# Optimization experiments

Hardware: AMD Instinct MI355X
Metric: run time of the kernel (lower is better)

Reference implementation:

```python
import jax, jax.numpy as jnp
import numpy as np

B, N, D = 8, 1024, 768
R, SH = 10, 2
H = R + SH            # 12 total heads
DH = D // H           # 64
DF = 2 * D            # FFN hidden


def _layernorm(x, g, b, eps=1e-5):
    mu = jnp.mean(x, axis=-1, keepdims=True)
    var = jnp.var(x, axis=-1, keepdims=True)
    return (x - mu) * jax.lax.rsqrt(var + eps) * g + b


def setup_inputs() -> dict:
    key = jax.random.key(0)
    ks = jax.random.split(key, 12)
    s = 0.02
    inp = {
        'nodes': jax.random.normal(ks[0], (B, N, D), dtype=jnp.float32),
        'relation_mask': jax.random.uniform(ks[1], (B, N, N, R), dtype=jnp.float32),
        'node_mask': jax.random.randint(ks[2], (B, N), 0, 2).astype(bool),
        'Wq': jax.random.normal(ks[3], (D, D), dtype=jnp.float32) * s,
        'bq': jnp.zeros((D,), jnp.float32),
        'Wk': jax.random.normal(ks[4], (D, D), dtype=jnp.float32) * s,
        'bk': jnp.zeros((D,), jnp.float32),
        'Wv': jax.random.normal(ks[5], (D, D), dtype=jnp.float32) * s,
        'bv': jnp.zeros((D,), jnp.float32),
        'Wo': jax.random.normal(ks[6], (D, D), dtype=jnp.float32) * s,
        'bo': jnp.zeros((D,), jnp.float32),
        'ln1_g': jnp.ones((D,), jnp.float32),
        'ln1_b': jnp.zeros((D,), jnp.float32),
        'W1': jax.random.normal(ks[7], (DF, D), dtype=jnp.float32) * s,
        'b1': jnp.zeros((DF,), jnp.float32),
        'W2': jax.random.normal(ks[8], (D, DF), dtype=jnp.float32) * s,
        'b2': jnp.zeros((D,), jnp.float32),
        'ln2_g': jnp.ones((D,), jnp.float32),
        'ln2_b': jnp.zeros((D,), jnp.float32),
    }
    return inp


def reference(nodes, relation_mask, node_mask, Wq, bq, Wk, bk, Wv, bv, Wo, bo,
              ln1_g, ln1_b, W1, b1, W2, b2, ln2_g, ln2_b):
    neg_inf = jnp.float32(-jnp.inf)
    # projections -> [B, H, N, DH]
    q = (nodes @ Wq.T + bq).reshape(B, N, H, DH).transpose(0, 2, 1, 3)
    k = (nodes @ Wk.T + bk).reshape(B, N, H, DH).transpose(0, 2, 1, 3)
    v = (nodes @ Wv.T + bv).reshape(B, N, H, DH).transpose(0, 2, 1, 3)
    scores = jnp.einsum('bhqd,bhkd->bhqk', q, k) / jnp.sqrt(jnp.float32(DH))
    # relation-typed gating on first R heads
    rel_gate = relation_mask.transpose(0, 3, 1, 2)          # [B, R, N, N]
    typed = jnp.where(rel_gate < 1e-4, neg_inf, scores[:, :R])
    scores = jnp.concatenate([typed, scores[:, R:]], axis=1)
    # key padding mask
    key_mask = node_mask[:, None, None, :]                  # [B,1,1,N]
    scores = jnp.where(key_mask, scores, neg_inf)
    attn = jax.nn.softmax(scores, axis=-1)
    attn = jnp.nan_to_num(attn, nan=0.0)                    # rows with no valid keys -> 0
    out = jnp.einsum('bhqk,bhkd->bhqd', attn, v)
    out = out.transpose(0, 2, 1, 3).reshape(B, N, D)
    out = out @ Wo.T + bo
    h = _layernorm(nodes + out, ln1_g, ln1_b)
    ffn = jax.nn.gelu(h @ W1.T + b1, approximate=False) @ W2.T + b2
    h = _layernorm(h + ffn, ln2_g, ln2_b)
    return h
```

## Files before the change

### kernel.cpp

```cpp
#include <hip/hip_runtime.h>
#include <stdint.h>
#include <math.h>

typedef unsigned short u16;
typedef __bf16 bf16x8 __attribute__((ext_vector_type(8)));
typedef unsigned short u16x8 __attribute__((ext_vector_type(8)));
typedef unsigned short us4 __attribute__((ext_vector_type(4)));
typedef float f32x4 __attribute__((ext_vector_type(4)));

#define DEVI __device__ __forceinline__

constexpr int B_ = 8, N_ = 1024, D_ = 768, H_ = 12, DH_ = 64, DF_ = 1536;

DEVI u16 f2bu(float f) {
  unsigned x = __builtin_bit_cast(unsigned, f);
  x += 0x7FFFu + ((x >> 16) & 1u);
  return (u16)(x >> 16);
}

DEVI bf16x8 ld_frag(const u16* p) {
  return __builtin_bit_cast(bf16x8, *(const u16x8*)p);
}

DEVI void gload_lds16(const u16* g, u16* l) {
  __builtin_amdgcn_global_load_lds(
      (const __attribute__((address_space(1))) void*)g,
      (__attribute__((address_space(3))) void*)l, 16, 0, 0);
}

struct CvtArgs {
  const float* src[7];
  u16* dst[7];
  int n4[7];
  int start[8];
};
__global__ __launch_bounds__(256)
void cvt_all(CvtArgs a) {
  const int gb = blockIdx.x;
  int j = 0;
  while (gb >= a.start[j + 1]) ++j;
  const int i = (gb - a.start[j]) * 256 + threadIdx.x;
  if (i >= a.n4[j]) return;
  float4 v = ((const float4*)a.src[j])[i];
  ushort4 o;
  o.x = f2bu(v.x); o.y = f2bu(v.y); o.z = f2bu(v.z); o.w = f2bu(v.w);
  ((ushort4*)a.dst[j])[i] = o;
}

__global__ __launch_bounds__(256)
void build_mask_packed(const float* __restrict__ rel, const int* __restrict__ nm,
                       u16* __restrict__ mp) {
  const int b = blockIdx.z, q0 = blockIdx.y * 16, k0 = blockIdx.x * 256;
  const int t = threadIdx.x;
  __shared__ u16 w12[16][256];
  const int key_ok = nm[(b << 10) + k0 + t];
  const float th = 1e-4f;
#pragma unroll 1
  for (int it = 0; it < 16; ++it) {
    unsigned bits;
    if (!key_ok) {
      bits = 0xFFFu;
    } else {
      const size_t idx = (((size_t)(b << 10) + q0 + it) << 10) + k0 + t;
      const float2* rp = (const float2*)(rel + idx * 10);
      float2 a0 = rp[0], a1 = rp[1], a2 = rp[2], a3 = rp[3], a4 = rp[4];
      bits  = (a0.x < th ? 1u : 0u)   | (a0.y < th ? 2u : 0u)
            | (a1.x < th ? 4u : 0u)   | (a1.y < th ? 8u : 0u)
            | (a2.x < th ? 16u : 0u)  | (a2.y < th ? 32u : 0u)
            | (a3.x < th ? 64u : 0u)  | (a3.y < th ? 128u : 0u)
            | (a4.x < th ? 256u : 0u) | (a4.y < th ? 512u : 0u);
    }
    w12[it][t ^ ((it & 7) << 1)] = (u16)bits;
  }
  __syncthreads();
  const int ql = t & 15, kt = t >> 4;
  unsigned wv[16];
#pragma unroll
  for (int j2 = 0; j2 < 8; ++j2) {
    const int e = (kt * 16 + j2 * 2) ^ ((ql & 7) << 1);
    wv[j2 * 2] = w12[ql][e];
    wv[j2 * 2 + 1] = w12[ql][e + 1];
  }
#pragma unroll
  for (int h = 0; h < 12; ++h) {
    unsigned word = 0;
#pragma unroll
    for (int j = 0; j < 16; ++j) word |= ((wv[j] >> h) & 1u) << j;
    mp[(((size_t)(b * H_ + h)) * (N_ / 16) + (k0 >> 4) + kt) * N_ + q0 + ql] = (u16)word;
  }
}

template<int EPI>
__global__ __launch_bounds__(256, 2)
void gemm_bt(const u16* __restrict__ A, const u16* __restrict__ Bm,
             const float* __restrict__ bias0, const float* __restrict__ bias1,
             const float* __restrict__ resid,
             u16* __restrict__ out0, u16* __restrict__ out1, float* __restrict__ outf,
             int M, int N, int K) {
  __shared__ u16 As[2][128 * 32];
  __shared__ u16 Bs[2][128 * 32];
  const int t = threadIdx.x;
  const int w = t >> 6, l = t & 63;
  const int li = l & 15, grp = l >> 4;
  const int nwg = gridDim.x * gridDim.y;
  int id = blockIdx.y * gridDim.x + blockIdx.x;
  id = (id & 7) * (nwg >> 3) + (id >> 3);
  const int by = id / gridDim.x;
  const int bx = id - by * gridDim.x;
  const int n0 = bx * 128, m0 = by * 128;
  const int wr = w >> 1, wc = w & 1;

  f32x4 acc[4][4] = {};

  const int arow = w * 16 + (l >> 2);
  const int acol = (l & 3) * 8;
  const u16* Ag = A + (size_t)(m0 + arow) * K + acol;
  const u16* Bg = Bm + (size_t)(n0 + arow) * K + acol;

  auto stage = [&](int buf, int k0) {
    u16* Asw = &As[buf][(w * 16) * 32];
    u16* Bsw = &Bs[buf][(w * 16) * 32];
    gload_lds16(Ag + k0, Asw);
    gload_lds16(Ag + (size_t)64 * K + k0, Asw + 64 * 32);
    gload_lds16(Bg + k0, Bsw);
    gload_lds16(Bg + (size_t)64 * K + k0, Bsw + 64 * 32);
  };

  stage(0, 0);
  __syncthreads();
  int cur = 0;
  for (int k0 = 0; k0 < K; k0 += 32) {
    if (k0 + 32 < K) stage(cur ^ 1, k0 + 32);
    bf16x8 af[4], bfr[4];
#pragma unroll
    for (int m = 0; m < 4; ++m)
      af[m] = ld_frag(&As[cur][(wr * 64 + m * 16 + li) * 32 + grp * 8]);
#pragma unroll
    for (int n = 0; n < 4; ++n)
      bfr[n] = ld_frag(&Bs[cur][(wc * 64 + n * 16 + li) * 32 + grp * 8]);
#pragma unroll
    for (int m = 0; m < 4; ++m)
#pragma unroll
      for (int n = 0; n < 4; ++n)
        acc[m][n] = __builtin_amdgcn_mfma_f32_16x16x32_bf16(af[m], bfr[n], acc[m][n], 0, 0, 0);
    __syncthreads();
    cur ^= 1;
  }

#pragma unroll
  for (int m = 0; m < 4; ++m) {
#pragma unroll
    for (int n = 0; n < 4; ++n) {
#pragma unroll
      for (int j = 0; j < 4; ++j) {
        const int row = m0 + wr * 64 + m * 16 + grp * 4 + j;
        const int col = n0 + wc * 64 + n * 16 + li;
        float v = acc[m][n][j];
        if constexpr (EPI == 0) {
          v += (col < D_) ? bias0[col] : bias1[col - D_];
          const int b = row >> 10, i = row & (N_ - 1);
          int c2 = (col < D_) ? col : col - D_;
          u16* dst = (col < D_) ? out0 : out1;
          dst[(((size_t)(b * H_ + (c2 >> 6))) * N_ + i) * DH_ + (c2 & 63)] = f2bu(v);
        } else if constexpr (EPI == 1) {
          v += bias0[row];
          const int b = col >> 10, i = col & (N_ - 1);
          out0[(((size_t)(b * H_ + (row >> 6))) * DH_ + (row & 63)) * N_ + i] = f2bu(v);
        } else if constexpr (EPI == 2) {
          v += bias0[col] + resid[(size_t)row * D_ + col];
          outf[(size_t)row * D_ + col] = v;
        } else {
          v += bias0[col];
          float gel = 0.5f * v * (1.0f + erff(v * 0.70710678118654752440f));
          out0[(size_t)row * DF_ + col] = f2bu(gel);
        }
      }
    }
  }
}

__global__ __launch_bounds__(512, 4)
void attn(const u16* __restrict__ q, const u16* __restrict__ k, const u16* __restrict__ vT,
          const u16* __restrict__ mp, u16* __restrict__ outp) {
  const int nwg = gridDim.x;
  const int p = blockIdx.x;
  const int lid = (p & 7) * (nwg >> 3) + (p >> 3);
  const int bh_i = lid >> 3;
  const int qblk = lid & 7;
  const int b = bh_i / H_, h = bh_i - (bh_i / H_) * H_;
  const int w = threadIdx.x >> 6, l = threadIdx.x & 63;
  const int li = l & 15, grp = l >> 4;
  const int qw = qblk * 128 + w * 16;
  const size_t bh = (size_t)bh_i;

  __shared__ u16 Kt[2][64 * 64];
  __shared__ u16 Vt[2][64 * 64];
  __shared__ u16 P[8][16 * 64];

  const u16* kbase = k + bh * N_ * DH_;
  const u16* vbase = vT + bh * DH_ * N_;

  const int srow_off = l >> 3;
  const int sg = l & 7;
  const int r0 = w * 8;
  auto stageK = [&](int buf, int kj0) {
    const int row = r0 + srow_off;
    const int gp = sg ^ (row & 7);
    gload_lds16(kbase + (size_t)(kj0 + row) * DH_ + gp * 8, &Kt[buf][r0 * 64]);
  };
  auto stageV = [&](int buf, int kj0) {
    const int row = r0 + srow_off;
    const int gp = sg ^ (row & 7);
    gload_lds16(vbase + (size_t)row * N_ + kj0 + gp * 8, &Vt[buf][r0 * 64]);
  };

  const u16* qp = q + (bh * N_ + qw) * DH_;
  const bf16x8 bq0 = ld_frag(qp + li * DH_ + grp * 8);
  const bf16x8 bq1 = ld_frag(qp + li * DH_ + 32 + grp * 8);

  f32x4 accO[4] = {};
  float m = -INFINITY, lsum = 0.f;

  u16* Pw = &P[w][0];
  const int sw = (li & 7) << 3;
  const int prow = li * 64;
  const u16* mrow = mp + bh * (N_ / 16) * N_ + qw + li;

  stageK(0, 0); stageV(0, 0);
  __syncthreads();
  int cur = 0;

  for (int kj0 = 0; kj0 < N_; kj0 += 64) {
    if (kj0 + 64 < N_) { stageK(cur ^ 1, kj0 + 64); stageV(cur ^ 1, kj0 + 64); }
    unsigned mword[4];
#pragma unroll
    for (int t = 0; t < 4; ++t) mword[t] = mrow[(size_t)((kj0 >> 4) + t) * N_];

    f32x4 s[4];
    __builtin_amdgcn_s_setprio(1);
#pragma unroll
    for (int t = 0; t < 4; ++t) {
      const int row = t * 16 + li;
      const int rs = row & 7;
      const bf16x8 ka0 = ld_frag(&Kt[cur][row * 64 + ((grp ^ rs) * 8)]);
      const bf16x8 ka1 = ld_frag(&Kt[cur][row * 64 + (((grp + 4) ^ rs) * 8)]);
      f32x4 z = {0.f, 0.f, 0.f, 0.f};
      z = __builtin_amdgcn_mfma_f32_16x16x32_bf16(ka0, bq0, z, 0, 0, 0);
      z = __builtin_amdgcn_mfma_f32_16x16x32_bf16(ka1, bq1, z, 0, 0, 0);
      s[t] = z;
    }
    __builtin_amdgcn_s_setprio(0);

    float pv[16];
    float rmax = -INFINITY;
#pragma unroll
    for (int t = 0; t < 4; ++t) {
      const unsigned mb = (mword[t] >> (grp * 4)) & 0xFu;
#pragma unroll
      for (int j = 0; j < 4; ++j) {
        const float sv = ((mb >> j) & 1u) ? -INFINITY : s[t][j] * 0.125f;
        pv[t * 4 + j] = sv;
        rmax = fmaxf(rmax, sv);
      }
    }
    rmax = fmaxf(rmax, __shfl_xor(rmax, 16));
    rmax = fmaxf(rmax, __shfl_xor(rmax, 32));
    const float mnew = fmaxf(m, rmax);
    const float scal = (mnew == m) ? 1.0f : __expf(m - mnew);
    float psum = 0.f;
#pragma unroll
    for (int i = 0; i < 16; ++i) {
      const float e = (pv[i] == -INFINITY) ? 0.0f : __expf(pv[i] - mnew);
      pv[i] = e;
      psum += e;
    }
    psum += __shfl_xor(psum, 16);
    psum += __shfl_xor(psum, 32);
    lsum = lsum * scal + psum;
    m = mnew;
#pragma unroll
    for (int t2 = 0; t2 < 4; ++t2) accO[t2] *= scal;
#pragma unroll
    for (int t = 0; t < 4; ++t) {
      us4 pk;
      pk[0] = f2bu(pv[t * 4 + 0]); pk[1] = f2bu(pv[t * 4 + 1]);
      pk[2] = f2bu(pv[t * 4 + 2]); pk[3] = f2bu(pv[t * 4 + 3]);
      *(us4*)&Pw[prow + ((t * 16 + grp * 4) ^ sw)] = pk;
    }
    __builtin_amdgcn_s_setprio(1);
#pragma unroll
    for (int kc = 0; kc < 2; ++kc) {
      const bf16x8 pb = ld_frag(&Pw[prow + ((kc * 32 + grp * 8) ^ sw)]);
#pragma unroll
      for (int t2 = 0; t2 < 4; ++t2) {
        const int row = t2 * 16 + li;
        const bf16x8 va = ld_frag(&Vt[cur][row * 64 + (((kc * 4 + grp) ^ (row & 7)) * 8)]);
        accO[t2] = __builtin_amdgcn_mfma_f32_16x16x32_bf16(va, pb, accO[t2], 0, 0, 0);
      }
    }
    __builtin_amdgcn_s_setprio(0);
    __syncthreads();
    cur ^= 1;
  }
  const float inv = (lsum > 0.f) ? 1.0f / lsum : 0.f;
  u16* op = outp + ((size_t)b * N_ + qw + li) * D_ + h * DH_;
#pragma unroll
  for (int t2 = 0; t2 < 4; ++t2) {
    us4 ov;
    ov[0] = f2bu(accO[t2][0] * inv); ov[1] = f2bu(accO[t2][1] * inv);
    ov[2] = f2bu(accO[t2][2] * inv); ov[3] = f2bu(accO[t2][3] * inv);
    *(us4*)&op[t2 * 16 + grp * 4] = ov;
  }
}

__global__ __launch_bounds__(256)
void ln_kernel(const float* __restrict__ x, const float* __restrict__ g,
               const float* __restrict__ be, float* __restrict__ y, u16* __restrict__ ybf) {
  const int row = blockIdx.x;
  const int t = threadIdx.x;
  const float* xr = x + (size_t)row * D_;
  const float v0 = xr[t], v1 = xr[t + 256], v2 = xr[t + 512];
  float s = v0 + v1 + v2;
  float s2 = v0 * v0 + v1 * v1 + v2 * v2;
#pragma unroll
  for (int d = 1; d < 64; d <<= 1) { s += __shfl_xor(s, d); s2 += __shfl_xor(s2, d); }
  __shared__ float red[8];
  const int w = t >> 6;
  if ((t & 63) == 0) { red[w] = s; red[4 + w] = s2; }
  __syncthreads();
  s = red[0] + red[1] + red[2] + red[3];
  s2 = red[4] + red[5] + red[6] + red[7];
  const float mu = s * (1.0f / D_);
  const float var = fmaxf(s2 * (1.0f / D_) - mu * mu, 0.0f);
  const float rstd = rsqrtf(var + 1e-5f);
  float* yr = y + (size_t)row * D_;
  u16* br = ybf ? ybf + (size_t)row * D_ : (u16*)nullptr;
  {
    float o = (v0 - mu) * rstd * g[t] + be[t];
    yr[t] = o; if (br) br[t] = f2bu(o);
  }
  {
    float o = (v1 - mu) * rstd * g[t + 256] + be[t + 256];
    yr[t + 256] = o; if (br) br[t + 256] = f2bu(o);
  }
  {
    float o = (v2 - mu) * rstd * g[t + 512] + be[t + 512];
    yr[t + 512] = o; if (br) br[t + 512] = f2bu(o);
  }
}

extern "C" void kernel_launch(void* const* d_in, const int* in_sizes, int n_in,
                              void* d_out, int out_size, void* d_ws, size_t ws_size,
                              hipStream_t stream) {
  (void)in_sizes; (void)n_in; (void)out_size; (void)ws_size;
  const float* nodes = (const float*)d_in[0];
  const float* rel   = (const float*)d_in[1];
  const int*   nmask = (const int*)d_in[2];
  const float* Wq = (const float*)d_in[3];
  const float* bq = (const float*)d_in[4];
  const float* Wk = (const float*)d_in[5];
  const float* bk = (const float*)d_in[6];
  const float* Wv = (const float*)d_in[7];
  const float* bv = (const float*)d_in[8];
  const float* Wo = (const float*)d_in[9];
  const float* bo = (const float*)d_in[10];
  const float* ln1g = (const float*)d_in[11];
  const float* ln1b = (const float*)d_in[12];
  const float* W1 = (const float*)d_in[13];
  const float* b1 = (const float*)d_in[14];
  const float* W2 = (const float*)d_in[15];
  const float* b2 = (const float*)d_in[16];
  const float* ln2g = (const float*)d_in[17];
  const float* ln2b = (const float*)d_in[18];
  float* out = (float*)d_out;

  char* ws = (char*)d_ws;
  u16* Wqk_bf = (u16*)(ws + 0);
  u16* Wv_bf  = (u16*)(ws + 2359296);
  u16* Wo_bf  = (u16*)(ws + 3538944);
  u16* W1_bf  = (u16*)(ws + 4718592);
  u16* W2_bf  = (u16*)(ws + 7077888);
  u16* Xbf    = (u16*)(ws + 9437184);
  u16* qb     = (u16*)(ws + 22020096);
  u16* kb     = (u16*)(ws + 34603008);
  u16* vTb    = (u16*)(ws + 47185920);
  u16* mwb    = (u16*)(ws + 59768832);
  float* preh = (float*)(ws + 22020096);
  u16* hbf    = (u16*)(ws + 47185920);
  u16* f1b    = (u16*)(ws + 59768832);
  float* preo = (float*)(ws + 84934656);
  u16* attno  = Xbf;

  const dim3 blk(256);
  CvtArgs ca;
  ca.src[0] = Wq; ca.src[1] = Wk; ca.src[2] = Wv; ca.src[3] = Wo;
  ca.src[4] = W1; ca.src[5] = W2; ca.src[6] = nodes;
  ca.dst[0] = Wqk_bf; ca.dst[1] = Wqk_bf + 768 * 768; ca.dst[2] = Wv_bf;
  ca.dst[3] = Wo_bf; ca.dst[4] = W1_bf; ca.dst[5] = W2_bf; ca.dst[6] = Xbf;
  ca.n4[0] = ca.n4[1] = ca.n4[2] = ca.n4[3] = 147456;
  ca.n4[4] = ca.n4[5] = 294912; ca.n4[6] = 1572864;
  ca.start[0] = 0; ca.start[1] = 576; ca.start[2] = 1152; ca.start[3] = 1728;
  ca.start[4] = 2304; ca.start[5] = 3456; ca.start[6] = 4608; ca.start[7] = 10752;
  cvt_all<<<10752, blk, 0, stream>>>(ca);
  build_mask_packed<<<dim3(4, 64, 8), blk, 0, stream>>>(rel, nmask, mwb);
  gemm_bt<0><<<dim3(12, 64), blk, 0, stream>>>(Xbf, Wqk_bf, bq, bk, nullptr,
                                               qb, kb, nullptr, 8192, 1536, 768);
  gemm_bt<1><<<dim3(64, 6), blk, 0, stream>>>(Wv_bf, Xbf, bv, nullptr, nullptr,
                                              vTb, nullptr, nullptr, 768, 8192, 768);
  attn<<<768, dim3(512), 0, stream>>>(qb, kb, vTb, mwb, attno);
  gemm_bt<2><<<dim3(6, 64), blk, 0, stream>>>(attno, Wo_bf, bo, nullptr, nodes,
                                              nullptr, nullptr, preh, 8192, 768, 768);
  ln_kernel<<<8192, blk, 0, stream>>>(preh, ln1g, ln1b, preh, hbf);
  gemm_bt<3><<<dim3(12, 64), blk, 0, stream>>>(hbf, W1_bf, b1, nullptr, nullptr,
                                               f1b, nullptr, nullptr, 8192, 1536, 768);
  gemm_bt<2><<<dim3(6, 64), blk, 0, stream>>>(f1b, W2_bf, b2, nullptr, preh,
                                              nullptr, nullptr, preo, 8192, 768, 1536);
  ln_kernel<<<8192, blk, 0, stream>>>(preo, ln2g, ln2b, out, nullptr);
}
```

Measured before the change: 347.9 us.

## Store pre-LN activations in bf16, fold softmax scale into Q, lazy rescale

Pre-layernorm residual sums are now stored as bf16 instead of fp32, and the second residual reads the bf16 LN1 output. This halves the intermediate traffic and drops the duplicate fp32 LN1 output. The 1/sqrt(dh) scale moves into the Q projection epilogue. The online softmax skips rescaling unless the running max grows by more than a threshold, which removes per-element -inf checks and exp calls. The mask build launch is also reordered before the weight conversion. The risk is reduced precision in the residual path and possible overflow margin in the lazy softmax.

```diff
diff --git a/kernel.cpp b/kernel.cpp
--- a/kernel.cpp
+++ b/kernel.cpp
@@ -17,6 +17,7 @@
   x += 0x7FFFu + ((x >> 16) & 1u);
   return (u16)(x >> 16);
 }
+DEVI float b2f(u16 u) { return __builtin_bit_cast(float, (unsigned)u << 16); }
 
 DEVI bf16x8 ld_frag(const u16* p) {
   return __builtin_bit_cast(bf16x8, *(const u16x8*)p);
@@ -94,8 +95,8 @@
 __global__ __launch_bounds__(256, 2)
 void gemm_bt(const u16* __restrict__ A, const u16* __restrict__ Bm,
              const float* __restrict__ bias0, const float* __restrict__ bias1,
-             const float* __restrict__ resid,
-             u16* __restrict__ out0, u16* __restrict__ out1, float* __restrict__ outf,
+             const float* __restrict__ residf, const u16* __restrict__ residb,
+             u16* __restrict__ out0, u16* __restrict__ out1,
              int M, int N, int K) {
   __shared__ u16 As[2][128 * 32];
   __shared__ u16 Bs[2][128 * 32];
@@ -158,6 +159,7 @@
         float v = acc[m][n][j];
         if constexpr (EPI == 0) {
           v += (col < D_) ? bias0[col] : bias1[col - D_];
+          if (col < D_) v *= 0.125f;
           const int b = row >> 10, i = row & (N_ - 1);
           int c2 = (col < D_) ? col : col - D_;
           u16* dst = (col < D_) ? out0 : out1;
@@ -167,12 +169,15 @@
           const int b = col >> 10, i = col & (N_ - 1);
           out0[(((size_t)(b * H_ + (row >> 6))) * DH_ + (row & 63)) * N_ + i] = f2bu(v);
         } else if constexpr (EPI == 2) {
-          v += bias0[col] + resid[(size_t)row * D_ + col];
-          outf[(size_t)row * D_ + col] = v;
-        } else {
+          v += bias0[col] + residf[(size_t)row * N + col];
+          out0[(size_t)row * N + col] = f2bu(v);
+        } else if constexpr (EPI == 3) {
           v += bias0[col];
           float gel = 0.5f * v * (1.0f + erff(v * 0.70710678118654752440f));
-          out0[(size_t)row * DF_ + col] = f2bu(gel);
+          out0[(size_t)row * N + col] = f2bu(gel);
+        } else {
+          v += bias0[col] + b2f(residb[(size_t)row * N + col]);
+          out0[(size_t)row * N + col] = f2bu(v);
         }
       }
     }
@@ -251,35 +256,40 @@
     }
     __builtin_amdgcn_s_setprio(0);
 
-    float pv[16];
+    float sv[16];
     float rmax = -INFINITY;
 #pragma unroll
     for (int t = 0; t < 4; ++t) {
       const unsigned mb = (mword[t] >> (grp * 4)) & 0xFu;
 #pragma unroll
       for (int j = 0; j < 4; ++j) {
-        const float sv = ((mb >> j) & 1u) ? -INFINITY : s[t][j] * 0.125f;
-        pv[t * 4 + j] = sv;
-        rmax = fmaxf(rmax, sv);
+        const float x = ((mb >> j) & 1u) ? -INFINITY : s[t][j];
+        sv[t * 4 + j] = x;
+        rmax = fmaxf(rmax, x);
       }
     }
     rmax = fmaxf(rmax, __shfl_xor(rmax, 16));
     rmax = fmaxf(rmax, __shfl_xor(rmax, 32));
-    const float mnew = fmaxf(m, rmax);
-    const float scal = (mnew == m) ? 1.0f : __expf(m - mnew);
+    if (!__all(rmax <= m + 8.f)) {
+      const float mnew = fmaxf(m, rmax);
+      const float scal = (m == -INFINITY) ? 0.f : __expf(m - mnew);
+      lsum *= scal;
+#pragma unroll
+      for (int t2 = 0; t2 < 4; ++t2) accO[t2] *= scal;
+      m = mnew;
+    }
+    const float msafe = (m == -INFINITY) ? 0.f : m;
     float psum = 0.f;
+    float pv[16];
 #pragma unroll
     for (int i = 0; i < 16; ++i) {
-      const float e = (pv[i] == -INFINITY) ? 0.0f : __expf(pv[i] - mnew);
+      const float e = __expf(sv[i] - msafe);
       pv[i] = e;
       psum += e;
     }
     psum += __shfl_xor(psum, 16);
     psum += __shfl_xor(psum, 32);
-    lsum = lsum * scal + psum;
-    m = mnew;
-#pragma unroll
-    for (int t2 = 0; t2 < 4; ++t2) accO[t2] *= scal;
+    lsum += psum;
 #pragma unroll
     for (int t = 0; t < 4; ++t) {
       us4 pk;
@@ -313,13 +323,15 @@
   }
 }
 
+template<int OUTF32>
 __global__ __launch_bounds__(256)
-void ln_kernel(const float* __restrict__ x, const float* __restrict__ g,
-               const float* __restrict__ be, float* __restrict__ y, u16* __restrict__ ybf) {
+void ln_kernel(const u16* __restrict__ x, const float* __restrict__ g,
+               const float* __restrict__ be, u16* __restrict__ ybf,
+               float* __restrict__ yf) {
   const int row = blockIdx.x;
   const int t = threadIdx.x;
-  const float* xr = x + (size_t)row * D_;
-  const float v0 = xr[t], v1 = xr[t + 256], v2 = xr[t + 512];
+  const u16* xr = x + (size_t)row * D_;
+  const float v0 = b2f(xr[t]), v1 = b2f(xr[t + 256]), v2 = b2f(xr[t + 512]);
   float s = v0 + v1 + v2;
   float s2 = v0 * v0 + v1 * v1 + v2 * v2;
 #pragma unroll
@@ -333,19 +345,13 @@
   const float mu = s * (1.0f / D_);
   const float var = fmaxf(s2 * (1.0f / D_) - mu * mu, 0.0f);
   const float rstd = rsqrtf(var + 1e-5f);
-  float* yr = y + (size_t)row * D_;
-  u16* br = ybf ? ybf + (size_t)row * D_ : (u16*)nullptr;
-  {
-    float o = (v0 - mu) * rstd * g[t] + be[t];
-    yr[t] = o; if (br) br[t] = f2bu(o);
-  }
-  {
-    float o = (v1 - mu) * rstd * g[t + 256] + be[t + 256];
-    yr[t + 256] = o; if (br) br[t + 256] = f2bu(o);
-  }
-  {
-    float o = (v2 - mu) * rstd * g[t + 512] + be[t + 512];
-    yr[t + 512] = o; if (br) br[t + 512] = f2bu(o);
+#pragma unroll
+  for (int c = 0; c < 3; ++c) {
+    const int idx = t + c * 256;
+    const float vv = (c == 0) ? v0 : (c == 1) ? v1 : v2;
+    const float o = (vv - mu) * rstd * g[idx] + be[idx];
+    if constexpr (OUTF32) yf[(size_t)row * D_ + idx] = o;
+    else ybf[(size_t)row * D_ + idx] = f2bu(o);
   }
 }
 
@@ -385,13 +391,14 @@
   u16* kb     = (u16*)(ws + 34603008);
   u16* vTb    = (u16*)(ws + 47185920);
   u16* mwb    = (u16*)(ws + 59768832);
-  float* preh = (float*)(ws + 22020096);
+  u16* prehb  = (u16*)(ws + 22020096);
   u16* hbf    = (u16*)(ws + 47185920);
   u16* f1b    = (u16*)(ws + 59768832);
-  float* preo = (float*)(ws + 84934656);
+  u16* preob  = (u16*)(ws + 84934656);
   u16* attno  = Xbf;
 
   const dim3 blk(256);
+  build_mask_packed<<<dim3(4, 64, 8), blk, 0, stream>>>(rel, nmask, mwb);
   CvtArgs ca;
   ca.src[0] = Wq; ca.src[1] = Wk; ca.src[2] = Wv; ca.src[3] = Wo;
   ca.src[4] = W1; ca.src[5] = W2; ca.src[6] = nodes;
@@ -402,18 +409,17 @@
   ca.start[0] = 0; ca.start[1] = 576; ca.start[2] = 1152; ca.start[3] = 1728;
   ca.start[4] = 2304; ca.start[5] = 3456; ca.start[6] = 4608; ca.start[7] = 10752;
   cvt_all<<<10752, blk, 0, stream>>>(ca);
-  build_mask_packed<<<dim3(4, 64, 8), blk, 0, stream>>>(rel, nmask, mwb);
-  gemm_bt<0><<<dim3(12, 64), blk, 0, stream>>>(Xbf, Wqk_bf, bq, bk, nullptr,
-                                               qb, kb, nullptr, 8192, 1536, 768);
-  gemm_bt<1><<<dim3(64, 6), blk, 0, stream>>>(Wv_bf, Xbf, bv, nullptr, nullptr,
-                                              vTb, nullptr, nullptr, 768, 8192, 768);
+  gemm_bt<0><<<dim3(12, 64), blk, 0, stream>>>(Xbf, Wqk_bf, bq, bk, nullptr, nullptr,
+                                               qb, kb, 8192, 1536, 768);
+  gemm_bt<1><<<dim3(64, 6), blk, 0, stream>>>(Wv_bf, Xbf, bv, nullptr, nullptr, nullptr,
+                                              vTb, nullptr, 768, 8192, 768);
   attn<<<768, dim3(512), 0, stream>>>(qb, kb, vTb, mwb, attno);
-  gemm_bt<2><<<dim3(6, 64), blk, 0, stream>>>(attno, Wo_bf, bo, nullptr, nodes,
-                                              nullptr, nullptr, preh, 8192, 768, 768);
-  ln_kernel<<<8192, blk, 0, stream>>>(preh, ln1g, ln1b, preh, hbf);
-  gemm_bt<3><<<dim3(12, 64), blk, 0, stream>>>(hbf, W1_bf, b1, nullptr, nullptr,
-                                               f1b, nullptr, nullptr, 8192, 1536, 768);
-  gemm_bt<2><<<dim3(6, 64), blk, 0, stream>>>(f1b, W2_bf, b2, nullptr, preh,
-                                              nullptr, nullptr, preo, 8192, 768, 1536);
-  ln_kernel<<<8192, blk, 0, stream>>>(preo, ln2g, ln2b, out, nullptr);
-}
+  gemm_bt<2><<<dim3(6, 64), blk, 0, stream>>>(attno, Wo_bf, bo, nullptr, nodes, nullptr,
+                                              prehb, nullptr, 8192, 768, 768);
+  ln_kernel<0><<<8192, blk, 0, stream>>>(prehb, ln1g, ln1b, hbf, nullptr);
+  gemm_bt<3><<<dim3(12, 64), blk, 0, stream>>>(hbf, W1_bf, b1, nullptr, nullptr, nullptr,
+                                               f1b, nullptr, 8192, 1536, 768);
+  gemm_bt<4><<<dim3(6, 64), blk, 0, stream>>>(f1b, W2_bf, b2, nullptr, nullptr, hbf,
+                                              preob, nullptr, 8192, 768, 1536);
+  ln_kernel<1><<<8192, blk, 0, stream>>>(preob, ln2g, ln2b, nullptr, out);
+}
```

Result: faster. 307.4 us (-11.6%).
